# Kernel optimization log

Measured on AMD Instinct MI355X. Metric: run time of the kernel, lower is better.

The kernel has to match this reference:

```python
import jax, jax.numpy as jnp
import numpy as np

B = 32768
Z_DIM = 64
X_DIM = 256
HIDDEN = 512
T = 8            # num_transforms
NBINS = 8
TAIL = 25.0
MULT = 3 * NBINS - 1   # widths + heights + interior derivatives = 23
MIN_W = 1e-3
MIN_H = 1e-3
MIN_D = 1e-3


def _masks():
    # MADE degrees (nflows, random_mask=False)
    d_in = np.arange(1, Z_DIM + 1)                      # input degrees 1..D
    h = np.arange(HIDDEN) % (Z_DIM - 1) + 1             # hidden degrees
    o = np.arange(Z_DIM * MULT) // MULT + 1             # output degrees, MULT contiguous per feature
    m1 = (h[:, None] >= d_in[None, :]).astype(np.float32)   # [H, D]
    m2 = (h[:, None] >= h[None, :]).astype(np.float32)      # [H, H]
    m3 = (o[:, None] > h[None, :]).astype(np.float32)       # [D*MULT, H] strict for output layer
    return jnp.asarray(m1), jnp.asarray(m2), jnp.asarray(m3)


def _rq_spline_fwd(z, uw, uh, ud):
    """Unconstrained rational-quadratic spline with linear tails (forward).
    z: [B, D]; uw/uh: [B, D, NBINS]; ud: [B, D, NBINS-1].
    Returns (outputs [B,D], logabsdet [B,D])."""
    const = np.log(np.exp(1.0 - MIN_D) - 1.0)
    pad = jnp.full(ud.shape[:-1] + (1,), const, ud.dtype)
    ud = jnp.concatenate([pad, ud, pad], axis=-1)       # [B, D, NBINS+1]

    widths = jax.nn.softmax(uw, axis=-1)
    widths = MIN_W + (1.0 - MIN_W * NBINS) * widths
    zero = jnp.zeros(widths.shape[:-1] + (1,), widths.dtype)
    cumw = jnp.concatenate([zero, jnp.cumsum(widths, axis=-1)], axis=-1)
    cumw = -TAIL + 2.0 * TAIL * cumw
    cumw = cumw.at[..., 0].set(-TAIL).at[..., -1].set(TAIL)
    widths = cumw[..., 1:] - cumw[..., :-1]

    derivs = MIN_D + jax.nn.softplus(ud)

    heights = jax.nn.softmax(uh, axis=-1)
    heights = MIN_H + (1.0 - MIN_H * NBINS) * heights
    cumh = jnp.concatenate([zero, jnp.cumsum(heights, axis=-1)], axis=-1)
    cumh = -TAIL + 2.0 * TAIL * cumh
    cumh = cumh.at[..., 0].set(-TAIL).at[..., -1].set(TAIL)
    heights = cumh[..., 1:] - cumh[..., :-1]

    delta = heights / widths

    z_in = jnp.clip(z, -TAIL, TAIL)
    edges = cumw.at[..., -1].add(1e-6)                  # nflows searchsorted eps
    idx = jnp.sum(z_in[..., None] >= edges, axis=-1) - 1
    idx = jnp.clip(idx, 0, NBINS - 1)

    g = lambda a: jnp.take_along_axis(a, idx[..., None], axis=-1)[..., 0]
    in_cw = g(cumw); in_w = g(widths)
    in_ch = g(cumh); in_h = g(heights)
    in_dl = g(delta)
    d0 = g(derivs); d1 = g(derivs[..., 1:])

    th = (z_in - in_cw) / in_w
    th1 = th * (1.0 - th)
    num = in_h * (in_dl * th * th + d0 * th1)
    den = in_dl + (d0 + d1 - 2.0 * in_dl) * th1
    out = in_ch + num / den
    dnum = in_dl ** 2 * (d1 * th * th + 2.0 * in_dl * th1 + d0 * (1.0 - th) ** 2)
    lad = jnp.log(dnum) - 2.0 * jnp.log(den)

    inside = (z >= -TAIL) & (z <= TAIL)
    return jnp.where(inside, out, z), jnp.where(inside, lad, 0.0)


def setup_inputs() -> dict:
    key = jax.random.key(0)
    ks = jax.random.split(key, 10)
    s = 0.05  # small init scale keeps spline params in a sane regime
    return {
        "z": jax.random.normal(ks[0], (B, Z_DIM), jnp.float32),
        "x": jax.random.normal(ks[1], (B, X_DIM), jnp.float32),
        "W1": jax.random.normal(ks[2], (T, HIDDEN, Z_DIM), jnp.float32) * s,
        "b1": jax.random.normal(ks[3], (T, HIDDEN), jnp.float32) * s,
        "Wc": jax.random.normal(ks[4], (T, HIDDEN, X_DIM), jnp.float32) * s,
        "bc": jax.random.normal(ks[5], (T, HIDDEN), jnp.float32) * s,
        "W2": jax.random.normal(ks[6], (T, HIDDEN, HIDDEN), jnp.float32) * s,
        "b2": jax.random.normal(ks[7], (T, HIDDEN), jnp.float32) * s,
        "W3": jax.random.normal(ks[8], (T, Z_DIM * MULT, HIDDEN), jnp.float32) * s,
        "b3": jax.random.normal(ks[9], (T, Z_DIM * MULT), jnp.float32) * s,
    }


def reference(z, x, W1, b1, Wc, bc, W2, b2, W3, b3):
    """log q(z|x) of the composed MADE-RQ-spline flow, shape [B]."""
    m1, m2, m3 = _masks()
    inv_sqrt_h = 1.0 / np.sqrt(HIDDEN)
    cur = z
    total_lad = jnp.zeros(z.shape[0], z.dtype)
    for t in range(T):
        # MADE: masked initial layer + context layer, one masked feedforward block (linear->relu), masked output layer
        h = cur @ (W1[t] * m1).T + b1[t] + x @ Wc[t].T + bc[t]
        h = jax.nn.relu(h @ (W2[t] * m2).T + b2[t])
        p = (h @ (W3[t] * m3).T + b3[t]).reshape(-1, Z_DIM, MULT)
        uw = p[..., :NBINS] * inv_sqrt_h
        uh = p[..., NBINS:2 * NBINS] * inv_sqrt_h
        ud = p[..., 2 * NBINS:]
        cur, lad = _rq_spline_fwd(cur, uw, uh, ud)
        total_lad = total_lad + lad.sum(axis=-1)
    log_base = -0.5 * jnp.sum(cur ** 2, axis=-1) - 0.5 * Z_DIM * np.log(2.0 * np.pi)
    return log_base + total_lad
```

## Files before the change

kernel.cpp:

```cpp
#include <hip/hip_runtime.h>
#include <cstdint>
#include <cstddef>

#define B_ROWS 32768
#define ZD 64
#define XD 256
#define HID 512
#define T_STEPS 8
#define MULT 23
#define MPAD 24
#define NOUT 1472
#define NPAD 1536
#define K1 320
#define PSTRIDE 200

typedef float f32x4 __attribute__((ext_vector_type(4)));
typedef short s16x8 __attribute__((ext_vector_type(8)));

__device__ __forceinline__ unsigned short f2bf(float f) {
  unsigned int u = __float_as_uint(f);
  u = (u + 0x7FFFu + ((u >> 16) & 1u)) >> 16;
  return (unsigned short)u;
}
__device__ __forceinline__ float bf2f(unsigned short s) {
  return __uint_as_float(((unsigned int)s) << 16);
}

__device__ __forceinline__ int permP(int n) {
  return (n < 72) ? (n / 9) + 63 * (n % 9)
                  : ((n - 72) >> 3) + 8 + 63 * ((n - 72) & 7);
}
__device__ __forceinline__ int degP(int n) {
  return (n < 72) ? (n / 9) + 1 : ((n - 72) >> 3) + 9;
}


__global__ void prep_weights(const float* __restrict__ W1, const float* __restrict__ Wc,
                             const float* __restrict__ W2, const float* __restrict__ W3,
                             const float* __restrict__ b1, const float* __restrict__ bc,
                             const float* __restrict__ b2, const float* __restrict__ b3,
                             unsigned short* __restrict__ w1c, unsigned short* __restrict__ w2c,
                             unsigned short* __restrict__ w3c,
                             float* __restrict__ ob1, float* __restrict__ ob2,
                             float* __restrict__ ob3) {
  const int S1 = T_STEPS * HID * K1;
  const int S2 = S1 + T_STEPS * HID * HID;
  const int S3 = S2 + T_STEPS * NPAD * HID;
  const int S4 = S3 + T_STEPS * HID;
  const int S5 = S4 + T_STEPS * HID;
  const int S6 = S5 + T_STEPS * NPAD;
  int i = blockIdx.x * 256 + threadIdx.x;
  if (i < S1) {
    int t = i / (HID * K1);
    int r = i - t * (HID * K1);
    int n = r / K1;
    int k = r - n * K1;
    int on = permP(n);
    float v;
    if (k < ZD) v = ((on % 63) >= k) ? W1[((size_t)t * HID + on) * ZD + k] : 0.0f;
    else        v = Wc[((size_t)t * HID + on) * XD + (k - ZD)];
    w1c[i] = f2bf(v);
  } else if (i < S2) {
    int j = i - S1;
    int t = j / (HID * HID);
    int r = j - t * (HID * HID);
    int n = r / HID;
    int k = r - n * HID;
    float v = 0.0f;
    if (degP(n) >= degP(k))
      v = W2[((size_t)t * HID + permP(n)) * HID + permP(k)];
    w2c[j] = f2bf(v);
  } else if (i < S3) {
    int j = i - S2;
    int t = j / (NPAD * HID);
    int r = j - t * (NPAD * HID);
    int n = r / HID;
    int k = r - n * HID;
    int d = n / MPAD;
    int jj = n - d * MPAD;
    float v = 0.0f;
    if (jj < MULT && d >= degP(k))
      v = W3[((size_t)t * NOUT + d * MULT + jj) * HID + permP(k)];
    w3c[j] = f2bf(v);
  } else if (i < S4) {
    int j = i - S3;
    int t = j / HID, n = j - t * HID;
    int on = permP(n);
    ob1[j] = b1[(size_t)t * HID + on] + bc[(size_t)t * HID + on];
  } else if (i < S5) {
    int j = i - S4;
    int t = j / HID, n = j - t * HID;
    ob2[j] = b2[(size_t)t * HID + permP(n)];
  } else if (i < S6) {
    int j = i - S5;
    int t = j / NPAD;
    int n = j - t * NPAD;
    int d = n / MPAD;
    int jj = n - d * MPAD;
    ob3[j] = (jj < MULT) ? b3[(size_t)t * NOUT + d * MULT + jj] : 0.0f;
  }
}

__global__ void prep_data(const float* __restrict__ x, const float* __restrict__ z,
                          unsigned short* __restrict__ A1,
                          float* __restrict__ curf, float* __restrict__ out) {
  const int SX = B_ROWS * XD;
  int i = blockIdx.x * 256 + threadIdx.x;
  if (i < SX) {
    int b = i >> 8;
    int j = i & 255;
    A1[(size_t)b * K1 + ZD + j] = f2bf(x[i]);
  } else {
    int j = i - SX;
    if (j < B_ROWS * ZD) {
      int b = j >> 6;
      int d = j & 63;
      float zv = z[j];
      A1[(size_t)b * K1 + d] = f2bf(zv);
      curf[j] = zv;
      if (d == 0) out[b] = -58.81206612509905f;
    }
  }
}


#define ASYNC16(gp, lp) __builtin_amdgcn_global_load_lds( \
    (__attribute__((address_space(1))) unsigned int*)(gp), \
    (__attribute__((address_space(3))) unsigned int*)(lp), 16, 0, 0)


__global__ __launch_bounds__(256, 3) void gemm_bias(
    const unsigned short* __restrict__ A,
    const unsigned short* __restrict__ Bw,
    const float* __restrict__ bias,
    unsigned short* __restrict__ C,
    int M, int N, int K, int relu, int tri)
{
  __shared__ alignas(16) unsigned short lA[2 * 128 * 32];
  __shared__ alignas(16) unsigned short lB[2 * 128 * 32];

  const int tid  = threadIdx.x;
  const int lane = tid & 63;
  const int wave = tid >> 6;

  const int lin = blockIdx.y * 4 + blockIdx.x;
  const int xcd = lin & 7;
  const int loc = lin >> 3;
  const int m0 = (xcd * 32 + (loc >> 2)) * 128;
  const int n0 = (loc & 3) * 128;
  const int Keff = tri ? min(K, 192 + n0) : K;

  const int wm = (wave >> 1) * 64;
  const int wn = (wave & 1) * 64;

  const int f    = tid * 16;
  const int row0 = f >> 6;
  const int colb = f & 63;

  char* gA0 = (char*)A  + ((size_t)(m0 + row0) * K) * 2 + colb;
  char* gA1 = gA0 + (size_t)64 * K * 2;
  char* gB0 = (char*)Bw + ((size_t)(n0 + row0) * K) * 2 + colb;
  char* gB1 = gB0 + (size_t)64 * K * 2;

  unsigned short* lA0 = lA + wave * 512;
  unsigned short* lA1 = lA + 2048 + wave * 512;
  unsigned short* lB0 = lB + wave * 512;
  unsigned short* lB1 = lB + 2048 + wave * 512;

  f32x4 acc[4][4];
#pragma unroll
  for (int i = 0; i < 4; i++)
#pragma unroll
    for (int j = 0; j < 4; j++) acc[i][j] = (f32x4){0.f, 0.f, 0.f, 0.f};

  const int fr = lane & 15;
  const int fk = (lane >> 4) * 8;

  for (int k0 = 0; k0 < Keff; k0 += 64) {
    ASYNC16(gA0, lA0);
    ASYNC16(gA1, lA1);
    ASYNC16(gB0, lB0);
    ASYNC16(gB1, lB1);
    ASYNC16(gA0 + 64, lA0 + 4096);
    ASYNC16(gA1 + 64, lA1 + 4096);
    ASYNC16(gB0 + 64, lB0 + 4096);
    ASYNC16(gB1 + 64, lB1 + 4096);
    gA0 += 128; gA1 += 128; gB0 += 128; gB1 += 128;
    __syncthreads();

    s16x8 a0[4], b0[4], a1[4], b1[4];
#pragma unroll
    for (int i = 0; i < 4; i++) {
      a0[i] = *(const s16x8*)(lA + (wm + i * 16 + fr) * 32 + fk);
      a1[i] = *(const s16x8*)(lA + 4096 + (wm + i * 16 + fr) * 32 + fk);
    }
#pragma unroll
    for (int j = 0; j < 4; j++) {
      b0[j] = *(const s16x8*)(lB + (wn + j * 16 + fr) * 32 + fk);
      b1[j] = *(const s16x8*)(lB + 4096 + (wn + j * 16 + fr) * 32 + fk);
    }

#pragma unroll
    for (int i = 0; i < 4; i++)
#pragma unroll
      for (int j = 0; j < 4; j++)
        acc[i][j] = __builtin_amdgcn_mfma_f32_16x16x32_bf16(a0[i], b0[j], acc[i][j], 0, 0, 0);
#pragma unroll
    for (int i = 0; i < 4; i++)
#pragma unroll
      for (int j = 0; j < 4; j++)
        acc[i][j] = __builtin_amdgcn_mfma_f32_16x16x32_bf16(a1[i], b1[j], acc[i][j], 0, 0, 0);
    __syncthreads();
  }

#pragma unroll
  for (int j = 0; j < 4; j++) {
    const int col = n0 + wn + j * 16 + fr;
    const float bv = bias[col];
#pragma unroll
    for (int i = 0; i < 4; i++) {
      const int rbase = m0 + wm + i * 16 + (lane >> 4) * 4;
#pragma unroll
      for (int r = 0; r < 4; r++) {
        float v = acc[i][j][r] + bv;
        if (relu) v = fmaxf(v, 0.0f);
        C[(size_t)(rbase + r) * N + col] = f2bf(v);
      }
    }
  }
}


__device__ __forceinline__ void rq_spline(const unsigned short* __restrict__ pp,
                                          float zv, float& zn, float& lad) {
  const float TAILC = 25.0f;
  const float MIN_WC = 0.001f;
  const float MIN_DC = 0.001f;
  const float SCALE2 = 0.06376007120095582f;
  const float LN2 = 0.6931471805599453f;

  s16x8 vw = *(const s16x8*)(pp);
  s16x8 vh = *(const s16x8*)(pp + 8);
  s16x8 vd = *(const s16x8*)(pp + 16);

  bool inside = (zv >= -TAILC) && (zv <= TAILC);
  float z_in = fminf(fmaxf(zv, -TAILC), TAILC);

  float ew[8], eh[8], sw = 0.f, sh = 0.f;
#pragma unroll
  for (int i = 0; i < 8; i++) {
    ew[i] = exp2f(bf2f((unsigned short)vw[i]) * SCALE2); sw += ew[i];
  }
#pragma unroll
  for (int i = 0; i < 8; i++) {
    eh[i] = exp2f(bf2f((unsigned short)vh[i]) * SCALE2); sh += eh[i];
  }
  float iw = (1.0f - 8.0f * MIN_WC) / sw;
  float ih = (1.0f - 8.0f * MIN_WC) / sh;

  float cumw[9], cumh[9];
  cumw[0] = -TAILC; cumh[0] = -TAILC;
  float cw = 0.f, ch = 0.f;
#pragma unroll
  for (int i = 0; i < 8; i++) {
    cw += MIN_WC + ew[i] * iw;
    ch += MIN_WC + eh[i] * ih;
    cumw[i + 1] = fmaf(2.0f * TAILC, cw, -TAILC);
    cumh[i + 1] = fmaf(2.0f * TAILC, ch, -TAILC);
  }
  cumw[8] = TAILC; cumh[8] = TAILC;

  int idx = 0;
#pragma unroll
  for (int i = 1; i < 8; i++) idx += (z_in >= cumw[i]) ? 1 : 0;

  float in_cw = 0.f, cw1 = 1.f, in_ch = 0.f, ch1 = 1.f, u0 = 0.f, u1 = 0.f;
#pragma unroll
  for (int i = 0; i < 8; i++) {
    if (i == idx) {
      in_cw = cumw[i]; cw1 = cumw[i + 1];
      in_ch = cumh[i]; ch1 = cumh[i + 1];
      u0 = (i > 0) ? bf2f((unsigned short)vd[i - 1]) : 0.0f;
      u1 = (i < 7) ? bf2f((unsigned short)vd[i]) : 0.0f;
    }
  }
  float dd0 = (idx == 0) ? 1.0f
            : MIN_DC + fmaxf(u0, 0.f) + __logf(1.0f + __expf(-fabsf(u0)));
  float dd1 = (idx == 7) ? 1.0f
            : MIN_DC + fmaxf(u1, 0.f) + __logf(1.0f + __expf(-fabsf(u1)));
  float in_w = cw1 - in_cw;
  float in_h = ch1 - in_ch;

  float delta = in_h / in_w;
  float th  = (z_in - in_cw) / in_w;
  float th1 = th * (1.0f - th);
  float th2 = th * th;
  float num = in_h * (delta * th2 + dd0 * th1);
  float den = delta + (dd0 + dd1 - 2.0f * delta) * th1;
  float outz = in_ch + num / den;
  float omt = 1.0f - th;
  float dnum = delta * delta * (dd1 * th2 + 2.0f * delta * th1 + dd0 * omt * omt);
  float l = LN2 * (__log2f(dnum) - 2.0f * __log2f(den));

  zn  = inside ? outz : zv;
  lad = inside ? l : 0.0f;
}


__global__ __launch_bounds__(256, 2) void gemm3_spline(
    const unsigned short* __restrict__ A,
    const unsigned short* __restrict__ Bw,
    const float* __restrict__ bias,
    float* __restrict__ curf,
    unsigned short* __restrict__ A1,
    float* __restrict__ out,
    int last)
{
  __shared__ alignas(16) union {
    struct { unsigned short A[2 * 128 * 32]; unsigned short B[2 * 192 * 32]; } g;
    unsigned short p[128 * PSTRIDE];
  } sm;

  const int tid  = threadIdx.x;
  const int lane = tid & 63;
  const int wave = tid >> 6;

  const int lin = blockIdx.y * 8 + blockIdx.x;
  const int xcd = lin & 7;
  const int loc = lin >> 3;
  const int m0 = (xcd * 32 + (loc >> 3)) * 128;
  const int bn = loc & 7;
  const int n0 = bn * 192;
  const int Keff = 64 * (bn + 1);

  const int wm = (wave >> 1) * 64;
  const int wn = (wave & 1) * 96;
  const int fr = lane & 15;
  const int fk = (lane >> 4) * 8;

  const int srow = tid & 127;
  const int sb = m0 + srow;
  const int dl0 = (tid >> 7) * 4;
  const int d0 = bn * 8 + dl0;
  float4 cz = *(const float4*)(curf + (size_t)sb * ZD + d0);
  float bv[6];
#pragma unroll
  for (int j = 0; j < 6; j++) bv[j] = bias[n0 + wn + j * 16 + fr];

  const int f    = tid * 16;
  const int row0 = f >> 6;
  const int colb = f & 63;
  const int K = HID;

  char* gA0 = (char*)A  + ((size_t)(m0 + row0) * K) * 2 + colb;
  char* gA1 = gA0 + (size_t)64 * K * 2;
  char* gB0 = (char*)Bw + ((size_t)(n0 + row0) * K) * 2 + colb;
  char* gB1 = gB0 + (size_t)64 * K * 2;
  char* gB2 = gB1 + (size_t)64 * K * 2;

  unsigned short* lA0 = sm.g.A + wave * 512;
  unsigned short* lA1 = sm.g.A + 2048 + wave * 512;
  unsigned short* lB0 = sm.g.B + wave * 512;
  unsigned short* lB1 = sm.g.B + 2048 + wave * 512;
  unsigned short* lB2 = sm.g.B + 4096 + wave * 512;

  f32x4 acc[4][6];
#pragma unroll
  for (int i = 0; i < 4; i++)
#pragma unroll
    for (int j = 0; j < 6; j++) acc[i][j] = (f32x4){0.f, 0.f, 0.f, 0.f};

  for (int k0 = 0; k0 < Keff; k0 += 64) {
    ASYNC16(gA0, lA0);
    ASYNC16(gA1, lA1);
    ASYNC16(gB0, lB0);
    ASYNC16(gB1, lB1);
    ASYNC16(gB2, lB2);
    ASYNC16(gA0 + 64, lA0 + 4096);
    ASYNC16(gA1 + 64, lA1 + 4096);
    ASYNC16(gB0 + 64, lB0 + 6144);
    ASYNC16(gB1 + 64, lB1 + 6144);
    ASYNC16(gB2 + 64, lB2 + 6144);
    gA0 += 128; gA1 += 128; gB0 += 128; gB1 += 128; gB2 += 128;
    __syncthreads();

    s16x8 a0[4], a1[4], b0[6], b1[6];
#pragma unroll
    for (int i = 0; i < 4; i++) {
      a0[i] = *(const s16x8*)(sm.g.A + (wm + i * 16 + fr) * 32 + fk);
      a1[i] = *(const s16x8*)(sm.g.A + 4096 + (wm + i * 16 + fr) * 32 + fk);
    }
#pragma unroll
    for (int j = 0; j < 6; j++) {
      b0[j] = *(const s16x8*)(sm.g.B + (wn + j * 16 + fr) * 32 + fk);
      b1[j] = *(const s16x8*)(sm.g.B + 6144 + (wn + j * 16 + fr) * 32 + fk);
    }

#pragma unroll
    for (int i = 0; i < 4; i++)
#pragma unroll
      for (int j = 0; j < 6; j++)
        acc[i][j] = __builtin_amdgcn_mfma_f32_16x16x32_bf16(a0[i], b0[j], acc[i][j], 0, 0, 0);
#pragma unroll
    for (int i = 0; i < 4; i++)
#pragma unroll
      for (int j = 0; j < 6; j++)
        acc[i][j] = __builtin_amdgcn_mfma_f32_16x16x32_bf16(a1[i], b1[j], acc[i][j], 0, 0, 0);
    __syncthreads();
  }

#pragma unroll
  for (int j = 0; j < 6; j++) {
    const int col = wn + j * 16 + fr;
#pragma unroll
    for (int i = 0; i < 4; i++) {
      const int rbase = wm + i * 16 + (lane >> 4) * 4;
#pragma unroll
      for (int r = 0; r < 4; r++)
        sm.p[(rbase + r) * PSTRIDE + col] = f2bf(acc[i][j][r] + bv[j]);
    }
  }
  __syncthreads();

  const unsigned short* pp = sm.p + srow * PSTRIDE + dl0 * MPAD;
  float zn0, zn1, zn2, zn3, l0, l1, l2, l3;
  rq_spline(pp,            cz.x, zn0, l0);
  rq_spline(pp + MPAD,     cz.y, zn1, l1);
  rq_spline(pp + 2 * MPAD, cz.z, zn2, l2);
  rq_spline(pp + 3 * MPAD, cz.w, zn3, l3);

  *(float4*)(curf + (size_t)sb * ZD + d0) = make_float4(zn0, zn1, zn2, zn3);
  union { unsigned int u[2]; unsigned short s[4]; } pk;
  pk.s[0] = f2bf(zn0); pk.s[1] = f2bf(zn1); pk.s[2] = f2bf(zn2); pk.s[3] = f2bf(zn3);
  *(uint2*)(A1 + (size_t)sb * K1 + d0) = make_uint2(pk.u[0], pk.u[1]);

  float contrib = l0 + l1 + l2 + l3;
  if (last)
    contrib -= 0.5f * (zn0 * zn0 + zn1 * zn1 + zn2 * zn2 + zn3 * zn3);
  atomicAdd(&out[sb], contrib);
}


extern "C" void kernel_launch(void* const* d_in, const int* in_sizes, int n_in,
                              void* d_out, int out_size, void* d_ws, size_t ws_size,
                              hipStream_t stream)
{
  const float* z  = (const float*)d_in[0];
  const float* x  = (const float*)d_in[1];
  const float* W1 = (const float*)d_in[2];
  const float* b1 = (const float*)d_in[3];
  const float* Wc = (const float*)d_in[4];
  const float* bc = (const float*)d_in[5];
  const float* W2 = (const float*)d_in[6];
  const float* b2 = (const float*)d_in[7];
  const float* W3 = (const float*)d_in[8];
  const float* b3 = (const float*)d_in[9];
  float* out = (float*)d_out;
  char* ws = (char*)d_ws;

  size_t oA1 = 0;
  size_t oH1 = oA1 + (size_t)B_ROWS * K1 * 2;
  size_t oH2 = oH1 + (size_t)B_ROWS * HID * 2;
  size_t oCU = oH2 + (size_t)B_ROWS * HID * 2;
  size_t oW1 = oCU + (size_t)B_ROWS * ZD * 4;
  size_t oW2 = oW1 + (size_t)T_STEPS * HID * K1 * 2;
  size_t oW3 = oW2 + (size_t)T_STEPS * HID * HID * 2;
  size_t oB1 = oW3 + (size_t)T_STEPS * NPAD * HID * 2;
  size_t oB2 = oB1 + (size_t)T_STEPS * HID * 4;
  size_t oB3 = oB2 + (size_t)T_STEPS * HID * 4;

  unsigned short* A1  = (unsigned short*)(ws + oA1);
  unsigned short* h1  = (unsigned short*)(ws + oH1);
  unsigned short* h2  = (unsigned short*)(ws + oH2);
  float* curf = (float*)(ws + oCU);
  unsigned short* w1c = (unsigned short*)(ws + oW1);
  unsigned short* w2c = (unsigned short*)(ws + oW2);
  unsigned short* w3c = (unsigned short*)(ws + oW3);
  float* b1c = (float*)(ws + oB1);
  float* b2p = (float*)(ws + oB2);
  float* b3c = (float*)(ws + oB3);

  const int prepw_total = T_STEPS * (HID * K1 + HID * HID + NPAD * HID + 2 * HID + NPAD);
  prep_weights<<<(prepw_total + 255) / 256, 256, 0, stream>>>(
      W1, Wc, W2, W3, b1, bc, b2, b3, w1c, w2c, w3c, b1c, b2p, b3c);
  const int prepd_total = B_ROWS * (XD + ZD);
  prep_data<<<(prepd_total + 255) / 256, 256, 0, stream>>>(x, z, A1, curf, out);

  for (int t = 0; t < T_STEPS; ++t) {
    gemm_bias<<<dim3(4, B_ROWS / 128), 256, 0, stream>>>(
        A1, w1c + (size_t)t * HID * K1, b1c + (size_t)t * HID, h1,
        B_ROWS, HID, K1, 0, 0);
    gemm_bias<<<dim3(4, B_ROWS / 128), 256, 0, stream>>>(
        h1, w2c + (size_t)t * HID * HID, b2p + (size_t)t * HID, h2,
        B_ROWS, HID, HID, 1, 1);
    gemm3_spline<<<dim3(8, B_ROWS / 128), 256, 0, stream>>>(
        h2, w3c + (size_t)t * NPAD * HID, b3c + (size_t)t * NPAD,
        curf, A1, out, (t == T_STEPS - 1) ? 1 : 0);
  }
}
```

Baseline: 968.6 us.

## Double-buffer LDS staging in gemm3 K loop to overlap loads with MFMA

```diff
diff --git a/kernel.cpp b/kernel.cpp
--- a/kernel.cpp
+++ b/kernel.cpp
@@ -317,7 +317,7 @@
     int last)
 {
   __shared__ alignas(16) union {
-    struct { unsigned short A[2 * 128 * 32]; unsigned short B[2 * 192 * 32]; } g;
+    unsigned short stage[2][20480];
     unsigned short p[128 * PSTRIDE];
   } sm;
 
@@ -331,7 +331,7 @@
   const int m0 = (xcd * 32 + (loc >> 3)) * 128;
   const int bn = loc & 7;
   const int n0 = bn * 192;
-  const int Keff = 64 * (bn + 1);
+  const int nIter = bn + 1;
 
   const int wm = (wave >> 1) * 64;
   const int wn = (wave & 1) * 96;
@@ -358,42 +358,47 @@
   char* gB1 = gB0 + (size_t)64 * K * 2;
   char* gB2 = gB1 + (size_t)64 * K * 2;
 
-  unsigned short* lA0 = sm.g.A + wave * 512;
-  unsigned short* lA1 = sm.g.A + 2048 + wave * 512;
-  unsigned short* lB0 = sm.g.B + wave * 512;
-  unsigned short* lB1 = sm.g.B + 2048 + wave * 512;
-  unsigned short* lB2 = sm.g.B + 4096 + wave * 512;
-
   f32x4 acc[4][6];
 #pragma unroll
   for (int i = 0; i < 4; i++)
 #pragma unroll
     for (int j = 0; j < 6; j++) acc[i][j] = (f32x4){0.f, 0.f, 0.f, 0.f};
 
-  for (int k0 = 0; k0 < Keff; k0 += 64) {
-    ASYNC16(gA0, lA0);
-    ASYNC16(gA1, lA1);
-    ASYNC16(gB0, lB0);
-    ASYNC16(gB1, lB1);
-    ASYNC16(gB2, lB2);
-    ASYNC16(gA0 + 64, lA0 + 4096);
-    ASYNC16(gA1 + 64, lA1 + 4096);
-    ASYNC16(gB0 + 64, lB0 + 6144);
-    ASYNC16(gB1 + 64, lB1 + 6144);
-    ASYNC16(gB2 + 64, lB2 + 6144);
-    gA0 += 128; gA1 += 128; gB0 += 128; gB1 += 128; gB2 += 128;
-    __syncthreads();
-
+#define STAGE3(buf) do { \
+    unsigned short* sa  = sm.stage[buf] + wave * 512; \
+    unsigned short* sbp = sm.stage[buf] + 8192 + wave * 512; \
+    ASYNC16(gA0, sa); \
+    ASYNC16(gA1, sa + 2048); \
+    ASYNC16(gB0, sbp); \
+    ASYNC16(gB1, sbp + 2048); \
+    ASYNC16(gB2, sbp + 4096); \
+    ASYNC16(gA0 + 64, sa + 4096); \
+    ASYNC16(gA1 + 64, sa + 6144); \
+    ASYNC16(gB0 + 64, sbp + 6144); \
+    ASYNC16(gB1 + 64, sbp + 8192); \
+    ASYNC16(gB2 + 64, sbp + 10240); \
+    gA0 += 128; gA1 += 128; gB0 += 128; gB1 += 128; gB2 += 128; \
+  } while (0)
+
+  STAGE3(0);
+  __syncthreads();
+
+  int cur = 0;
+  for (int k = 0; k < nIter; ++k) {
+    if (k + 1 < nIter) STAGE3(cur ^ 1);
+
+    const unsigned short* ca = sm.stage[cur];
+    const unsigned short* cb = ca + 8192;
     s16x8 a0[4], a1[4], b0[6], b1[6];
 #pragma unroll
     for (int i = 0; i < 4; i++) {
-      a0[i] = *(const s16x8*)(sm.g.A + (wm + i * 16 + fr) * 32 + fk);
-      a1[i] = *(const s16x8*)(sm.g.A + 4096 + (wm + i * 16 + fr) * 32 + fk);
+      a0[i] = *(const s16x8*)(ca + (wm + i * 16 + fr) * 32 + fk);
+      a1[i] = *(const s16x8*)(ca + 4096 + (wm + i * 16 + fr) * 32 + fk);
     }
 #pragma unroll
     for (int j = 0; j < 6; j++) {
-      b0[j] = *(const s16x8*)(sm.g.B + (wn + j * 16 + fr) * 32 + fk);
-      b1[j] = *(const s16x8*)(sm.g.B + 6144 + (wn + j * 16 + fr) * 32 + fk);
+      b0[j] = *(const s16x8*)(cb + (wn + j * 16 + fr) * 32 + fk);
+      b1[j] = *(const s16x8*)(cb + 6144 + (wn + j * 16 + fr) * 32 + fk);
     }
 
 #pragma unroll
@@ -406,8 +411,11 @@
 #pragma unroll
       for (int j = 0; j < 6; j++)
         acc[i][j] = __builtin_amdgcn_mfma_f32_16x16x32_bf16(a1[i], b1[j], acc[i][j], 0, 0, 0);
+
     __syncthreads();
-  }
+    cur ^= 1;
+  }
+#undef STAGE3
 
 #pragma unroll
   for (int j = 0; j < 6; j++) {
```

Measured after the change: 1.001 ms. 1.03x slower.
